# Kernel tuning notes

Hardware: AMD Instinct MI355X
Metric: run time of the kernel (lower is better)

Reference implementation:

```python
import jax, jax.numpy as jnp
import numpy as np

N, E, NS, NB = 25000, 400000, 4, 8
S0, V0 = 64, 32            # input: 64x0e + 32x1o
MS, MV = 96, 96            # message irreps: 96x0e + 96x1o
OS, OV = 128, 32           # post-linear_down/skip: (64+64)x0e + 32x1o
NIRR = S0 + V0             # node_feats.irreps.num_irreps = 96
AVG_NEIGH = 16.0
Y1 = float(np.sqrt(3.0 / (4.0 * np.pi)))  # integral-normalized l=1 SH coeff


def setup_inputs() -> dict:
    key = jax.random.key(0)
    k = jax.random.split(key, 15)
    return {
        'node_feats': jax.random.normal(k[0], (N, S0 + 3 * V0), jnp.float32),
        'vectors': jax.random.normal(k[1], (E, 3), jnp.float32),
        'rbf': jax.random.uniform(k[2], (E, NB), jnp.float32),
        'species': jax.random.randint(k[3], (N,), 0, NS, jnp.int32),
        'senders': jax.random.randint(k[4], (E,), 0, N, jnp.int32),
        'receivers': jax.random.randint(k[5], (E,), 0, N, jnp.int32),
        'W_up_s': jax.random.normal(k[6], (S0, S0), jnp.float32),
        'W_up_v': jax.random.normal(k[7], (V0, V0), jnp.float32),
        'W_mlp1': jax.random.normal(k[8], (NB, 64), jnp.float32),
        'W_mlp2': jax.random.normal(k[9], (64, 64), jnp.float32),
        'W_mlp3': jax.random.normal(k[10], (64, MS + MV), jnp.float32),
        'W_down_s': jax.random.normal(k[11], (MS, OS), jnp.float32),
        'W_down_v': jax.random.normal(k[12], (MV, OV), jnp.float32),
        'W_skip_s': jax.random.normal(k[13], (NS, S0, OS), jnp.float32),
        'W_skip_v': jax.random.normal(k[14], (NS, V0, OV), jnp.float32),
    }


def reference(node_feats, vectors, rbf, species, senders, receivers,
              W_up_s, W_up_v, W_mlp1, W_mlp2, W_mlp3,
              W_down_s, W_down_v, W_skip_s, W_skip_v):
    n = node_feats.shape[0]
    s = node_feats[:, :S0]                      # [N, 64]   0e
    v = node_feats[:, S0:].reshape(n, V0, 3)    # [N, 32,3] 1o

    # linear_up (per-irrep linear, 1/sqrt(fan_in) path normalization), then gather
    s_up = (s @ W_up_s) * (1.0 / jnp.sqrt(S0))
    v_up = jnp.einsum('nci,cd->ndi', v, W_up_v) * (1.0 / jnp.sqrt(V0))
    s_e = s_up[senders]                         # [E, 64]
    v_e = v_up[senders]                         # [E, 32, 3]

    # spherical harmonics l=1, normalize=True, 'integral' normalization
    y = Y1 * vectors / (jnp.linalg.norm(vectors, axis=-1, keepdims=True) + 1e-12)

    # tensor products filtered to output irreps + 0e
    tp_v = s_e[:, :, None] * y[:, None, :]                       # 0e x 1o -> 1o [E,64,3]
    tp_s = jnp.einsum('eci,ei->ec', v_e, y) * (1.0 / jnp.sqrt(3.0))  # 1o x 1o -> 0e [E,32]
    msg_s = jnp.concatenate([s_e, tp_s], axis=1)                 # [E, 96]
    msg_v = jnp.concatenate([v_e, tp_v], axis=1)                 # [E, 96, 3]

    # radial MLP -> per-edge, per-irrep mixing weights
    h = jax.nn.silu(rbf @ W_mlp1 * (1.0 / jnp.sqrt(NB)))
    h = jax.nn.silu(h @ W_mlp2 * (1.0 / 8.0))
    mix = h @ W_mlp3 * (1.0 / 8.0)                               # [E, 192]

    inv = 1.0 / NIRR
    msg_s = msg_s * mix[:, :MS] * inv
    msg_v = msg_v * (mix[:, MS:] * inv)[:, :, None]

    # scatter-sum to receivers, then normalize by sqrt(avg_num_neighbors)
    agg_s = jax.ops.segment_sum(msg_s, receivers, num_segments=n) / jnp.sqrt(AVG_NEIGH)
    agg_v = jax.ops.segment_sum(msg_v, receivers, num_segments=n) / jnp.sqrt(AVG_NEIGH)

    # linear_down to 128x0e + 32x1o
    out_s = agg_s @ W_down_s * (1.0 / jnp.sqrt(MS))
    out_v = jnp.einsum('nci,cd->ndi', agg_v, W_down_v) * (1.0 / jnp.sqrt(MV))

    # species-indexed skip connection (indexed linear)
    skip_s = jnp.einsum('nc,ncd->nd', s, W_skip_s[species]) * (1.0 / jnp.sqrt(S0))
    skip_v = jnp.einsum('nci,ncd->ndi', v, W_skip_v[species]) * (1.0 / jnp.sqrt(V0))

    f_s = out_s + skip_s                                         # [N, 128]
    f_v = out_v + skip_v                                         # [N, 32, 3]

    # equivariant gate: first 96 scalars activated, last 32 scalars gate the vectors
    act_s = jax.nn.silu(f_s[:, :OS - OV])
    gates = jax.nn.silu(f_s[:, OS - OV:])
    gated_v = f_v * gates[:, :, None]
    return jnp.concatenate([act_s, gated_v.reshape(n, OV * 3)], axis=1)  # [N, 192]
```

## Files before the change

kernel.cpp:

```cpp
#include <hip/hip_runtime.h>
#include <hip/hip_bf16.h>
#include <hip/hip_fp16.h>
#include <hip/hip_fp8.h>

#define NN 25000
#define EE 400000

#define SC_UP_S 0.125f
#define SC_UP_V 0.17677669529663689f
#define Y1C 0.48860251190291992f
#define SC_MLP1 0.35355339059327373f
#define SC_MLP2 0.125f
#define SC3 0.0013020833333333333f
#define INV_SQRT3 0.57735026918962584f
#define SC_DOWN 0.025515518153991442f
#define SC_SKIP_S 0.125f
#define SC_SKIP_V 0.17677669529663689f

typedef __attribute__((ext_vector_type(8))) short short8;
typedef __attribute__((ext_vector_type(4))) float f32x4;

__device__ __forceinline__ float silu(float x) {
  return __fdividef(x, 1.f + __expf(-x));
}
__device__ __forceinline__ unsigned short f2bf(float f) {
  unsigned u = __float_as_uint(f);
  unsigned r = u + 0x7FFF + ((u >> 16) & 1);
  return (unsigned short)(r >> 16);
}
__device__ __forceinline__ float bf2f(unsigned short s) {
  return __uint_as_float(((unsigned)s) << 16);
}
__device__ __forceinline__ float bfe(short8 v, int idx) {
  return __uint_as_float(((unsigned)(unsigned short)v[idx]) << 16);
}
__device__ __forceinline__ unsigned packbf(float lo, float hi) {
  return ((unsigned)f2bf(hi) << 16) | (unsigned)f2bf(lo);
}
__device__ __forceinline__ unsigned char f2fp8(float x) {
  __hip_fp8_e4m3 v(x);
  return (unsigned char)v.__x;
}
__device__ __forceinline__ float fp82f(unsigned b) {
  __hip_fp8_e4m3 t;
  t.__x = (__hip_fp8_storage_t)b;
  return (float)t;
}

#define W_W1P 0
#define W_W2P 1024
#define W_W3B 3072
#define W_WDS 9216
#define W_WDV 15360
#define W_SUPB 16896
#define W_VUPB (W_SUPB + NN * 32)
#define W_DEG (W_VUPB + NN * 48)
#define W_PRE (W_DEG + NN)
#define W_CUR (W_PRE + NN + 8)
#define W_SRT (W_CUR + NN)
#define W_EDN (W_SRT + EE * 2)
#define W_END (W_EDN + EE * 56)

__global__ __launch_bounds__(256) void transpose_weights(
    const float* __restrict__ W1, const float* __restrict__ W2,
    const float* __restrict__ W3, const float* __restrict__ Wds,
    const float* __restrict__ Wdv, float* __restrict__ ws) {
  int t = blockIdx.x * 256 + threadIdx.x;
  int stride = gridDim.x * 256;
  unsigned short* W1p = (unsigned short*)(ws + W_W1P);
  unsigned short* W2p = (unsigned short*)(ws + W_W2P);
  unsigned short* W3b = (unsigned short*)(ws + W_W3B);
  unsigned short* Wdsb = (unsigned short*)(ws + W_WDS);
  unsigned short* Wdvb = (unsigned short*)(ws + W_WDV);
  for (int i = t; i < 2048; i += stride) {
    int c = i >> 5, k = i & 31;
    W1p[i] = (k < 8) ? f2bf(W1[k * 64 + c] * SC_MLP1) : (unsigned short)0;
  }
  for (int i = t; i < 4096; i += stride) {
    int c = i >> 6, k = i & 63;
    W2p[i] = f2bf(W2[k * 64 + c] * SC_MLP2);
  }
  for (int i = t; i < 12288; i += stride) {
    int c = i >> 6, k = i & 63;
    float sc = (c >= 64 && c < 96) ? (SC3 * INV_SQRT3) : SC3;
    W3b[i] = f2bf(W3[k * 192 + c] * sc);
  }
  for (int i = t; i < 12288; i += stride) {
    int o = i / 96, k = i - 96 * o;
    Wdsb[i] = f2bf(Wds[k * 128 + o] * SC_DOWN);
  }
  for (int i = t; i < 3072; i += stride) {
    int o = i / 96, k = i - 96 * o;
    Wdvb[i] = f2bf(Wdv[k * 32 + o] * SC_DOWN);
  }
}

__global__ __launch_bounds__(256) void up_kernel(
    const float* __restrict__ nf, const float* __restrict__ Wus,
    const float* __restrict__ Wuv, unsigned short* __restrict__ s_upb,
    unsigned short* __restrict__ v_upb) {
  int n = blockIdx.x;
  int t = threadIdx.x;
  __shared__ float sv[160];
  if (t < 160) sv[t] = nf[n * 160 + t];
  __syncthreads();
  if (t < 64) {
    float a = 0.f;
#pragma unroll
    for (int k = 0; k < 64; k++) a += sv[k] * Wus[k * 64 + t];
    s_upb[n * 64 + t] = f2bf(a * SC_UP_S);
  } else if (t < 160) {
    int j = t - 64;
    int c = j / 3, i = j - 3 * c;
    float a = 0.f;
#pragma unroll
    for (int k = 0; k < 32; k++) a += sv[64 + k * 3 + i] * Wuv[k * 32 + c];
    v_upb[n * 96 + j] = f2bf(a * SC_UP_V);
  }
}

__global__ __launch_bounds__(256) void count_deg(
    const int* __restrict__ receivers, int* __restrict__ deg) {
  int e = blockIdx.x * 256 + threadIdx.x;
  if (e < EE) atomicAdd(&deg[receivers[e]], 1);
}

__global__ __launch_bounds__(1024) void scan_kernel(
    const int* __restrict__ deg, int* __restrict__ prefix,
    int* __restrict__ cursor) {
  __shared__ int waveSums[16];
  __shared__ int sCarry;
  int t = threadIdx.x;
  int lane = t & 63, wv = t >> 6;
  if (t == 0) sCarry = 0;
  __syncthreads();
  for (int base = 0; base < NN; base += 1024) {
    int i = base + t;
    int x = (i < NN) ? deg[i] : 0;
    int v = x;
#pragma unroll
    for (int d = 1; d < 64; d <<= 1) {
      int u = __shfl_up(v, d, 64);
      if (lane >= d) v += u;
    }
    if (lane == 63) waveSums[wv] = v;
    __syncthreads();
    if (wv == 0 && lane < 16) {
      int s = waveSums[lane];
#pragma unroll
      for (int d = 1; d < 16; d <<= 1) {
        int u = __shfl_up(s, d, 64);
        if (lane >= d) s += u;
      }
      waveSums[lane] = s;
    }
    __syncthreads();
    int waveOff = (wv == 0) ? 0 : waveSums[wv - 1];
    int incl = v + waveOff + sCarry;
    if (i < NN) {
      prefix[i] = incl - x;
      cursor[i] = incl - x;
    }
    __syncthreads();
    if (t == 1023) sCarry = incl;
    __syncthreads();
  }
  if (t == 0) prefix[NN] = sCarry;
}

__global__ __launch_bounds__(256) void scatter_kernel(
    const int* __restrict__ senders, const int* __restrict__ receivers,
    int* __restrict__ cursor, int2* __restrict__ sorted) {
  int e = blockIdx.x * 256 + threadIdx.x;
  if (e < EE) {
    int r = receivers[e];
    int pos = atomicAdd(&cursor[r], 1);
    sorted[pos] = make_int2(e, senders[e]);
  }
}

__global__ __launch_bounds__(256, 4) void edge_down3(
    const float* __restrict__ rbf, const float* __restrict__ vectors,
    const int2* __restrict__ sorted,
    const unsigned short* __restrict__ W1p,
    const unsigned short* __restrict__ W2p,
    const unsigned short* __restrict__ W3b,
    const unsigned short* __restrict__ Wdsb,
    const unsigned short* __restrict__ Wdvb,
    const unsigned short* __restrict__ s_upb,
    const unsigned short* __restrict__ v_upb,
    unsigned char* __restrict__ edown) {
  __shared__ unsigned short sH[64 * 72];
  __shared__ unsigned short sMix[64 * 200];

  int t = threadIdx.x;
  int pbase = blockIdx.x * 64;
  int lane = t & 63;
  int wv = t >> 6;
  int rl = lane & 15;
  int kgrp = lane >> 4;
  int arow = 16 * wv + rl;
  int crow = 16 * wv + kgrp * 4;

  union S8 { short8 v; unsigned u[4]; };

  int2 es = sorted[pbase + arow];
  int eid = es.x, snd = es.y;
  const unsigned short* seb = s_upb + (size_t)snd * 64;
  const unsigned short* veb = v_upb + (size_t)snd * 96;
  short8 se0 = *(const short8*)&seb[kgrp * 8];
  short8 se1 = *(const short8*)&seb[32 + kgrp * 8];
  short8 ve0 = *(const short8*)&veb[24 * kgrp];
  short8 ve1 = *(const short8*)&veb[24 * kgrp + 8];
  short8 ve2 = *(const short8*)&veb[24 * kgrp + 16];
  float vx = vectors[(size_t)eid * 3 + 0];
  float vy = vectors[(size_t)eid * 3 + 1];
  float vz = vectors[(size_t)eid * 3 + 2];
  float nrm = sqrtf(vx * vx + vy * vy + vz * vz) + 1e-12f;
  float ysc = Y1C / nrm;
  float y0 = vx * ysc, y1 = vy * ysc, y2 = vz * ysc;

  S8 a1;
  a1.u[0] = a1.u[1] = a1.u[2] = a1.u[3] = 0u;
  if (kgrp == 0) {
    float4 ra = *(const float4*)(rbf + (size_t)eid * 8);
    float4 rb = *(const float4*)(rbf + (size_t)eid * 8 + 4);
    a1.u[0] = packbf(ra.x, ra.y);
    a1.u[1] = packbf(ra.z, ra.w);
    a1.u[2] = packbf(rb.x, rb.y);
    a1.u[3] = packbf(rb.z, rb.w);
  }
#pragma unroll
  for (int ct = 0; ct < 4; ct++) {
    short8 b = *(const short8*)&W1p[(ct * 16 + rl) * 32 + kgrp * 8];
    f32x4 acc = {0.f, 0.f, 0.f, 0.f};
    acc = __builtin_amdgcn_mfma_f32_16x16x32_bf16(a1.v, b, acc, 0, 0, 0);
#pragma unroll
    for (int rr = 0; rr < 4; rr++)
      sH[(crow + rr) * 72 + ct * 16 + rl] = f2bf(silu(acc[rr]));
  }

  {
    short8 a20 = *(const short8*)&sH[arow * 72 + kgrp * 8];
    short8 a21 = *(const short8*)&sH[arow * 72 + 32 + kgrp * 8];
#pragma unroll
    for (int ct = 0; ct < 4; ct++) {
      const unsigned short* wb = &W2p[(ct * 16 + rl) * 64];
      short8 b0 = *(const short8*)&wb[kgrp * 8];
      short8 b1 = *(const short8*)&wb[32 + kgrp * 8];
      f32x4 acc = {0.f, 0.f, 0.f, 0.f};
      acc = __builtin_amdgcn_mfma_f32_16x16x32_bf16(a20, b0, acc, 0, 0, 0);
      acc = __builtin_amdgcn_mfma_f32_16x16x32_bf16(a21, b1, acc, 0, 0, 0);
#pragma unroll
      for (int rr = 0; rr < 4; rr++)
        sH[(crow + rr) * 72 + ct * 16 + rl] = f2bf(silu(acc[rr]));
    }
  }

  {
    short8 a30 = *(const short8*)&sH[arow * 72 + kgrp * 8];
    short8 a31 = *(const short8*)&sH[arow * 72 + 32 + kgrp * 8];
#pragma unroll
    for (int nt = 0; nt < 12; nt++) {
      int cc = nt * 16 + rl;
      const unsigned short* wb = &W3b[cc * 64];
      short8 b0 = *(const short8*)&wb[kgrp * 8];
      short8 b1 = *(const short8*)&wb[32 + kgrp * 8];
      f32x4 acc = {0.f, 0.f, 0.f, 0.f};
      acc = __builtin_amdgcn_mfma_f32_16x16x32_bf16(a30, b0, acc, 0, 0, 0);
      acc = __builtin_amdgcn_mfma_f32_16x16x32_bf16(a31, b1, acc, 0, 0, 0);
#pragma unroll
      for (int rr = 0; rr < 4; rr++)
        sMix[(crow + rr) * 200 + cc] = f2bf(acc[rr]);
    }
  }

  const unsigned short* mrow = &sMix[arow * 200];
  S8 as0, as1, as2, mvp1, mvp2, mvp3;
  {
    short8 m = *(const short8*)&mrow[kgrp * 8];
#pragma unroll
    for (int q = 0; q < 4; q++)
      as0.u[q] = packbf(bfe(se0, 2 * q) * bfe(m, 2 * q),
                        bfe(se0, 2 * q + 1) * bfe(m, 2 * q + 1));
  }
  {
    short8 m = *(const short8*)&mrow[32 + kgrp * 8];
#pragma unroll
    for (int q = 0; q < 4; q++)
      as1.u[q] = packbf(bfe(se1, 2 * q) * bfe(m, 2 * q),
                        bfe(se1, 2 * q + 1) * bfe(m, 2 * q + 1));
  }
  {
    short8 m = *(const short8*)&mrow[64 + kgrp * 8];
#pragma unroll
    for (int q = 0; q < 4; q++) {
      float d0 = bfe(ve0, (6 * q) % 8 == 6 * q ? 6 * q : 6 * q) * 0.f;
      (void)d0;
      float e0, e1, e2, f0, f1, f2;
      if (6 * q < 8) e0 = bfe(ve0, 6 * q); else if (6 * q < 16) e0 = bfe(ve1, 6 * q - 8); else e0 = bfe(ve2, 6 * q - 16);
      if (6 * q + 1 < 8) e1 = bfe(ve0, 6 * q + 1); else if (6 * q + 1 < 16) e1 = bfe(ve1, 6 * q - 7); else e1 = bfe(ve2, 6 * q - 15);
      if (6 * q + 2 < 8) e2 = bfe(ve0, 6 * q + 2); else if (6 * q + 2 < 16) e2 = bfe(ve1, 6 * q - 6); else e2 = bfe(ve2, 6 * q - 14);
      if (6 * q + 3 < 8) f0 = bfe(ve0, 6 * q + 3); else if (6 * q + 3 < 16) f0 = bfe(ve1, 6 * q - 5); else f0 = bfe(ve2, 6 * q - 13);
      if (6 * q + 4 < 8) f1 = bfe(ve0, 6 * q + 4); else if (6 * q + 4 < 16) f1 = bfe(ve1, 6 * q - 4); else f1 = bfe(ve2, 6 * q - 12);
      if (6 * q + 5 < 8) f2 = bfe(ve0, 6 * q + 5); else if (6 * q + 5 < 16) f2 = bfe(ve1, 6 * q - 3); else f2 = bfe(ve2, 6 * q - 11);
      float da = e0 * y0 + e1 * y1 + e2 * y2;
      float db = f0 * y0 + f1 * y1 + f2 * y2;
      as2.u[q] = packbf(da * bfe(m, 2 * q), db * bfe(m, 2 * q + 1));
    }
  }
  mvp1.v = *(const short8*)&mrow[96 + kgrp * 8];
  mvp2.v = *(const short8*)&mrow[128 + kgrp * 8];
  mvp3.v = *(const short8*)&mrow[160 + kgrp * 8];
  __syncthreads();

  unsigned char* edL = (unsigned char*)sMix;
#pragma unroll
  for (int ot = 0; ot < 8; ot++) {
    int col = ot * 16 + rl;
    const unsigned short* wb = &Wdsb[col * 96];
    short8 b0 = *(const short8*)&wb[kgrp * 8];
    short8 b1 = *(const short8*)&wb[32 + kgrp * 8];
    short8 b2 = *(const short8*)&wb[64 + kgrp * 8];
    f32x4 acc = {0.f, 0.f, 0.f, 0.f};
    acc = __builtin_amdgcn_mfma_f32_16x16x32_bf16(as0.v, b0, acc, 0, 0, 0);
    acc = __builtin_amdgcn_mfma_f32_16x16x32_bf16(as1.v, b1, acc, 0, 0, 0);
    acc = __builtin_amdgcn_mfma_f32_16x16x32_bf16(as2.v, b2, acc, 0, 0, 0);
#pragma unroll
    for (int rr = 0; rr < 4; rr++)
      edL[(crow + rr) * 232 + col] = f2fp8(acc[rr]);
  }
  float yarr[3] = {y0, y1, y2};
#pragma unroll
  for (int i = 0; i < 3; i++) {
    S8 av0, av1, av2;
#pragma unroll
    for (int q = 0; q < 4; q++) {
      float g0, g1;
      {
        const int j0 = 0;
        (void)j0;
      }
      int ja = 6 * q + i, jb = 6 * q + 3 + i;
      if (ja < 8) g0 = bfe(ve0, ja); else if (ja < 16) g0 = bfe(ve1, ja - 8); else g0 = bfe(ve2, ja - 16);
      if (jb < 8) g1 = bfe(ve0, jb); else if (jb < 16) g1 = bfe(ve1, jb - 8); else g1 = bfe(ve2, jb - 16);
      av0.u[q] = packbf(g0 * bfe(mvp1.v, 2 * q), g1 * bfe(mvp1.v, 2 * q + 1));
      av1.u[q] = packbf(bfe(se0, 2 * q) * yarr[i] * bfe(mvp2.v, 2 * q),
                        bfe(se0, 2 * q + 1) * yarr[i] * bfe(mvp2.v, 2 * q + 1));
      av2.u[q] = packbf(bfe(se1, 2 * q) * yarr[i] * bfe(mvp3.v, 2 * q),
                        bfe(se1, 2 * q + 1) * yarr[i] * bfe(mvp3.v, 2 * q + 1));
    }
#pragma unroll
    for (int ot = 0; ot < 2; ot++) {
      int o = ot * 16 + rl;
      const unsigned short* wb = &Wdvb[o * 96];
      short8 b0 = *(const short8*)&wb[kgrp * 8];
      short8 b1 = *(const short8*)&wb[32 + kgrp * 8];
      short8 b2 = *(const short8*)&wb[64 + kgrp * 8];
      f32x4 acc = {0.f, 0.f, 0.f, 0.f};
      acc = __builtin_amdgcn_mfma_f32_16x16x32_bf16(av0.v, b0, acc, 0, 0, 0);
      acc = __builtin_amdgcn_mfma_f32_16x16x32_bf16(av1.v, b1, acc, 0, 0, 0);
      acc = __builtin_amdgcn_mfma_f32_16x16x32_bf16(av2.v, b2, acc, 0, 0, 0);
#pragma unroll
      for (int rr = 0; rr < 4; rr++)
        edL[(crow + rr) * 232 + 128 + o * 3 + i] = f2fp8(acc[rr]);
    }
  }
  __syncthreads();

  {
    int row = t >> 2, q = t & 3;
    const unsigned* src = (const unsigned*)(edL + row * 232 + q * 56);
    unsigned* dst = (unsigned*)(edown + (size_t)(pbase + row) * 224 + q * 56);
#pragma unroll
    for (int j = 0; j < 14; j++) dst[j] = src[j];
  }
}

__global__ __launch_bounds__(256) void gather_out3(
    const float* __restrict__ nf, const int* __restrict__ species,
    const int* __restrict__ prefix, const unsigned* __restrict__ edw,
    const float* __restrict__ Wss, const float* __restrict__ Wsv,
    float* __restrict__ out) {
  int n = blockIdx.x;
  int t = threadIdx.x;
  __shared__ float sNF[160];
  __shared__ float4 sPart[4][56];
  __shared__ float sEd[224];
  __shared__ float sF[224];
  if (t < 160) sNF[t] = nf[(size_t)n * 160 + t];
  int beg = prefix[n], end = prefix[n + 1];
  if (t < 224) {
    int u = t % 56, rg = t / 56;
    float a0 = 0.f, a1 = 0.f, a2 = 0.f, a3 = 0.f;
    for (int s = beg + rg; s < end; s += 4) {
      unsigned v = edw[(size_t)s * 56 + u];
      a0 += fp82f(v & 0xFF);
      a1 += fp82f((v >> 8) & 0xFF);
      a2 += fp82f((v >> 16) & 0xFF);
      a3 += fp82f(v >> 24);
    }
    sPart[rg][u] = make_float4(a0, a1, a2, a3);
  }
  __syncthreads();
  if (t < 56) {
    float4 a = sPart[0][t], b = sPart[1][t], c = sPart[2][t], d = sPart[3][t];
    sEd[4 * t + 0] = a.x + b.x + c.x + d.x;
    sEd[4 * t + 1] = a.y + b.y + c.y + d.y;
    sEd[4 * t + 2] = a.z + b.z + c.z + d.z;
    sEd[4 * t + 3] = a.w + b.w + c.w + d.w;
  }
  __syncthreads();
  int spec = species[n];
  if (t < 128) {
    const float* wsk = Wss + (size_t)spec * 64 * 128;
    float b = 0.f;
#pragma unroll
    for (int k = 0; k < 64; k++) b += sNF[k] * wsk[k * 128 + t];
    sF[t] = sEd[t] + b * SC_SKIP_S;
  } else if (t < 224) {
    int j = t - 128;
    int c = j / 3, i = j - 3 * c;
    const float* wsk = Wsv + (size_t)spec * 32 * 32;
    float b = 0.f;
#pragma unroll
    for (int k = 0; k < 32; k++) b += sNF[64 + k * 3 + i] * wsk[k * 32 + c];
    sF[t] = sEd[t] + b * SC_SKIP_V;
  }
  __syncthreads();
  if (t < 96) {
    out[(size_t)n * 192 + t] = silu(sF[t]);
  } else if (t < 192) {
    int j = t - 96;
    int c = j / 3;
    out[(size_t)n * 192 + t] = sF[128 + j] * silu(sF[96 + c]);
  }
}

extern "C" void kernel_launch(void* const* d_in, const int* in_sizes, int n_in,
                              void* d_out, int out_size, void* d_ws, size_t ws_size,
                              hipStream_t stream) {
  const float* nf = (const float*)d_in[0];
  const float* vectors = (const float*)d_in[1];
  const float* rbf = (const float*)d_in[2];
  const int* species = (const int*)d_in[3];
  const int* senders = (const int*)d_in[4];
  const int* receivers = (const int*)d_in[5];
  const float* Wus = (const float*)d_in[6];
  const float* Wuv = (const float*)d_in[7];
  const float* W1 = (const float*)d_in[8];
  const float* W2 = (const float*)d_in[9];
  const float* W3 = (const float*)d_in[10];
  const float* Wds = (const float*)d_in[11];
  const float* Wdv = (const float*)d_in[12];
  const float* Wss = (const float*)d_in[13];
  const float* Wsv = (const float*)d_in[14];

  float* ws = (float*)d_ws;
  const unsigned short* W1p = (const unsigned short*)(ws + W_W1P);
  const unsigned short* W2p = (const unsigned short*)(ws + W_W2P);
  const unsigned short* W3b = (const unsigned short*)(ws + W_W3B);
  const unsigned short* Wdsb = (const unsigned short*)(ws + W_WDS);
  const unsigned short* Wdvb = (const unsigned short*)(ws + W_WDV);
  unsigned short* s_upb = (unsigned short*)(ws + W_SUPB);
  unsigned short* v_upb = (unsigned short*)(ws + W_VUPB);
  int* deg = (int*)(ws + W_DEG);
  int* prefix = (int*)(ws + W_PRE);
  int* cursor = (int*)(ws + W_CUR);
  int2* sorted = (int2*)(ws + W_SRT);
  unsigned char* edown = (unsigned char*)(ws + W_EDN);
  float* out = (float*)d_out;

  transpose_weights<<<16, 256, 0, stream>>>(W1, W2, W3, Wds, Wdv, ws);
  up_kernel<<<NN, 256, 0, stream>>>(nf, Wus, Wuv, s_upb, v_upb);

  hipMemsetAsync(deg, 0, (size_t)NN * sizeof(int), stream);
  count_deg<<<(EE + 255) / 256, 256, 0, stream>>>(receivers, deg);
  scan_kernel<<<1, 1024, 0, stream>>>(deg, prefix, cursor);
  scatter_kernel<<<(EE + 255) / 256, 256, 0, stream>>>(senders, receivers,
                                                       cursor, sorted);
  edge_down3<<<EE / 64, 256, 0, stream>>>(rbf, vectors, sorted, W1p, W2p, W3b,
                                          Wdsb, Wdvb, s_upb, v_upb, edown);
  gather_out3<<<NN, 256, 0, stream>>>(nf, species, prefix, (const unsigned*)edown,
                                      Wss, Wsv, out);
}
```

Before: 355.9 us.

## Process edges in original order and scatter results by receiver rank

```diff
diff --git a/kernel.cpp b/kernel.cpp
--- a/kernel.cpp
+++ b/kernel.cpp
@@ -24,9 +24,8 @@
   return __fdividef(x, 1.f + __expf(-x));
 }
 __device__ __forceinline__ unsigned short f2bf(float f) {
-  unsigned u = __float_as_uint(f);
-  unsigned r = u + 0x7FFF + ((u >> 16) & 1);
-  return (unsigned short)(r >> 16);
+  __hip_bfloat16 h = __float2bfloat16(f);
+  return *reinterpret_cast<unsigned short*>(&h);
 }
 __device__ __forceinline__ float bf2f(unsigned short s) {
   return __uint_as_float(((unsigned)s) << 16);
@@ -52,19 +51,22 @@
 #define W_W3B 3072
 #define W_WDS 9216
 #define W_WDV 15360
-#define W_SUPB 16896
+#define W_WSS 16896
+#define W_WSV 33280
+#define W_SUPB 35328
 #define W_VUPB (W_SUPB + NN * 32)
 #define W_DEG (W_VUPB + NN * 48)
 #define W_PRE (W_DEG + NN)
 #define W_CUR (W_PRE + NN + 8)
-#define W_SRT (W_CUR + NN)
-#define W_EDN (W_SRT + EE * 2)
+#define W_RNK (W_CUR + NN)
+#define W_EDN (W_RNK + EE)
 #define W_END (W_EDN + EE * 56)
 
 __global__ __launch_bounds__(256) void transpose_weights(
     const float* __restrict__ W1, const float* __restrict__ W2,
     const float* __restrict__ W3, const float* __restrict__ Wds,
-    const float* __restrict__ Wdv, float* __restrict__ ws) {
+    const float* __restrict__ Wdv, const float* __restrict__ Wss,
+    const float* __restrict__ Wsv, float* __restrict__ ws) {
   int t = blockIdx.x * 256 + threadIdx.x;
   int stride = gridDim.x * 256;
   unsigned short* W1p = (unsigned short*)(ws + W_W1P);
@@ -72,6 +74,8 @@
   unsigned short* W3b = (unsigned short*)(ws + W_W3B);
   unsigned short* Wdsb = (unsigned short*)(ws + W_WDS);
   unsigned short* Wdvb = (unsigned short*)(ws + W_WDV);
+  unsigned short* Wssb = (unsigned short*)(ws + W_WSS);
+  unsigned short* Wsvb = (unsigned short*)(ws + W_WSV);
   for (int i = t; i < 2048; i += stride) {
     int c = i >> 5, k = i & 31;
     W1p[i] = (k < 8) ? f2bf(W1[k * 64 + c] * SC_MLP1) : (unsigned short)0;
@@ -93,6 +97,10 @@
     int o = i / 96, k = i - 96 * o;
     Wdvb[i] = f2bf(Wdv[k * 32 + o] * SC_DOWN);
   }
+  for (int i = t; i < 32768; i += stride)
+    Wssb[i] = f2bf(Wss[i] * SC_SKIP_S);
+  for (int i = t; i < 4096; i += stride)
+    Wsvb[i] = f2bf(Wsv[i] * SC_SKIP_V);
 }
 
 __global__ __launch_bounds__(256) void up_kernel(
@@ -168,20 +176,19 @@
   if (t == 0) prefix[NN] = sCarry;
 }
 
-__global__ __launch_bounds__(256) void scatter_kernel(
-    const int* __restrict__ senders, const int* __restrict__ receivers,
-    int* __restrict__ cursor, int2* __restrict__ sorted) {
+__global__ __launch_bounds__(256) void rank_kernel(
+    const int* __restrict__ receivers, int* __restrict__ cursor,
+    int* __restrict__ rankArr) {
   int e = blockIdx.x * 256 + threadIdx.x;
   if (e < EE) {
     int r = receivers[e];
-    int pos = atomicAdd(&cursor[r], 1);
-    sorted[pos] = make_int2(e, senders[e]);
-  }
-}
-
-__global__ __launch_bounds__(256, 4) void edge_down3(
+    rankArr[e] = atomicAdd(&cursor[r], 1);
+  }
+}
+
+__global__ __launch_bounds__(256, 4) void edge_down4(
     const float* __restrict__ rbf, const float* __restrict__ vectors,
-    const int2* __restrict__ sorted,
+    const int* __restrict__ senders, const int* __restrict__ rankArr,
     const unsigned short* __restrict__ W1p,
     const unsigned short* __restrict__ W2p,
     const unsigned short* __restrict__ W3b,
@@ -192,6 +199,7 @@
     unsigned char* __restrict__ edown) {
   __shared__ unsigned short sH[64 * 72];
   __shared__ unsigned short sMix[64 * 200];
+  __shared__ int sRank[64];
 
   int t = threadIdx.x;
   int pbase = blockIdx.x * 64;
@@ -204,8 +212,9 @@
 
   union S8 { short8 v; unsigned u[4]; };
 
-  int2 es = sorted[pbase + arow];
-  int eid = es.x, snd = es.y;
+  if (t < 64) sRank[t] = rankArr[pbase + t];
+  int eid = pbase + arow;
+  int snd = senders[eid];
   const unsigned short* seb = s_upb + (size_t)snd * 64;
   const unsigned short* veb = v_upb + (size_t)snd * 96;
   short8 se0 = *(const short8*)&seb[kgrp * 8];
@@ -295,8 +304,6 @@
     short8 m = *(const short8*)&mrow[64 + kgrp * 8];
 #pragma unroll
     for (int q = 0; q < 4; q++) {
-      float d0 = bfe(ve0, (6 * q) % 8 == 6 * q ? 6 * q : 6 * q) * 0.f;
-      (void)d0;
       float e0, e1, e2, f0, f1, f2;
       if (6 * q < 8) e0 = bfe(ve0, 6 * q); else if (6 * q < 16) e0 = bfe(ve1, 6 * q - 8); else e0 = bfe(ve2, 6 * q - 16);
       if (6 * q + 1 < 8) e1 = bfe(ve0, 6 * q + 1); else if (6 * q + 1 < 16) e1 = bfe(ve1, 6 * q - 7); else e1 = bfe(ve2, 6 * q - 15);
@@ -337,10 +344,6 @@
 #pragma unroll
     for (int q = 0; q < 4; q++) {
       float g0, g1;
-      {
-        const int j0 = 0;
-        (void)j0;
-      }
       int ja = 6 * q + i, jb = 6 * q + 3 + i;
       if (ja < 8) g0 = bfe(ve0, ja); else if (ja < 16) g0 = bfe(ve1, ja - 8); else g0 = bfe(ve2, ja - 16);
       if (jb < 8) g1 = bfe(ve0, jb); else if (jb < 16) g1 = bfe(ve1, jb - 8); else g1 = bfe(ve2, jb - 16);
@@ -371,61 +374,68 @@
   {
     int row = t >> 2, q = t & 3;
     const unsigned* src = (const unsigned*)(edL + row * 232 + q * 56);
-    unsigned* dst = (unsigned*)(edown + (size_t)(pbase + row) * 224 + q * 56);
+    unsigned* dst = (unsigned*)(edown + (size_t)sRank[row] * 224 + q * 56);
 #pragma unroll
     for (int j = 0; j < 14; j++) dst[j] = src[j];
   }
 }
 
-__global__ __launch_bounds__(256) void gather_out3(
+__global__ __launch_bounds__(256) void gather_out4(
     const float* __restrict__ nf, const int* __restrict__ species,
-    const int* __restrict__ prefix, const unsigned* __restrict__ edw,
-    const float* __restrict__ Wss, const float* __restrict__ Wsv,
-    float* __restrict__ out) {
+    const int* __restrict__ prefix, const unsigned char* __restrict__ edown,
+    const unsigned short* __restrict__ Wssb,
+    const unsigned short* __restrict__ Wsvb, float* __restrict__ out) {
   int n = blockIdx.x;
   int t = threadIdx.x;
   __shared__ float sNF[160];
-  __shared__ float4 sPart[4][56];
+  __shared__ float sPart[16 * 224];
   __shared__ float sEd[224];
   __shared__ float sF[224];
   if (t < 160) sNF[t] = nf[(size_t)n * 160 + t];
   int beg = prefix[n], end = prefix[n + 1];
   if (t < 224) {
-    int u = t % 56, rg = t / 56;
-    float a0 = 0.f, a1 = 0.f, a2 = 0.f, a3 = 0.f;
-    for (int s = beg + rg; s < end; s += 4) {
-      unsigned v = edw[(size_t)s * 56 + u];
-      a0 += fp82f(v & 0xFF);
-      a1 += fp82f((v >> 8) & 0xFF);
-      a2 += fp82f((v >> 16) & 0xFF);
-      a3 += fp82f(v >> 24);
-    }
-    sPart[rg][u] = make_float4(a0, a1, a2, a3);
-  }
-  __syncthreads();
-  if (t < 56) {
-    float4 a = sPart[0][t], b = sPart[1][t], c = sPart[2][t], d = sPart[3][t];
-    sEd[4 * t + 0] = a.x + b.x + c.x + d.x;
-    sEd[4 * t + 1] = a.y + b.y + c.y + d.y;
-    sEd[4 * t + 2] = a.z + b.z + c.z + d.z;
-    sEd[4 * t + 3] = a.w + b.w + c.w + d.w;
+    int u = t % 14, rg = t / 14;
+    float a[16];
+#pragma unroll
+    for (int j = 0; j < 16; j++) a[j] = 0.f;
+    for (int s = beg + rg; s < end; s += 16) {
+      uint4 v = *(const uint4*)(edown + (size_t)s * 224 + u * 16);
+      unsigned w[4] = {v.x, v.y, v.z, v.w};
+#pragma unroll
+      for (int p = 0; p < 4; p++) {
+        a[4 * p + 0] += fp82f(w[p] & 0xFF);
+        a[4 * p + 1] += fp82f((w[p] >> 8) & 0xFF);
+        a[4 * p + 2] += fp82f((w[p] >> 16) & 0xFF);
+        a[4 * p + 3] += fp82f(w[p] >> 24);
+      }
+    }
+#pragma unroll
+    for (int j = 0; j < 16; j += 4)
+      *(float4*)&sPart[rg * 224 + u * 16 + j] = *(float4*)&a[j];
+  }
+  __syncthreads();
+  if (t < 224) {
+    float s = 0.f;
+#pragma unroll
+    for (int rg = 0; rg < 16; rg++) s += sPart[rg * 224 + t];
+    sEd[t] = s;
   }
   __syncthreads();
   int spec = species[n];
   if (t < 128) {
-    const float* wsk = Wss + (size_t)spec * 64 * 128;
+    const unsigned short* wsk = Wssb + (size_t)spec * 8192;
     float b = 0.f;
 #pragma unroll
-    for (int k = 0; k < 64; k++) b += sNF[k] * wsk[k * 128 + t];
-    sF[t] = sEd[t] + b * SC_SKIP_S;
+    for (int k = 0; k < 64; k++) b += sNF[k] * bf2f(wsk[k * 128 + t]);
+    sF[t] = sEd[t] + b;
   } else if (t < 224) {
     int j = t - 128;
     int c = j / 3, i = j - 3 * c;
-    const float* wsk = Wsv + (size_t)spec * 32 * 32;
+    const unsigned short* wsk = Wsvb + (size_t)spec * 1024;
     float b = 0.f;
 #pragma unroll
-    for (int k = 0; k < 32; k++) b += sNF[64 + k * 3 + i] * wsk[k * 32 + c];
-    sF[t] = sEd[t] + b * SC_SKIP_V;
+    for (int k = 0; k < 32; k++) b += sNF[64 + k * 3 + i] * bf2f(wsk[k * 32 + c]);
+    sF[t] = sEd[t] + b;
   }
   __syncthreads();
   if (t < 96) {
@@ -462,25 +472,27 @@
   const unsigned short* W3b = (const unsigned short*)(ws + W_W3B);
   const unsigned short* Wdsb = (const unsigned short*)(ws + W_WDS);
   const unsigned short* Wdvb = (const unsigned short*)(ws + W_WDV);
+  const unsigned short* Wssb = (const unsigned short*)(ws + W_WSS);
+  const unsigned short* Wsvb = (const unsigned short*)(ws + W_WSV);
   unsigned short* s_upb = (unsigned short*)(ws + W_SUPB);
   unsigned short* v_upb = (unsigned short*)(ws + W_VUPB);
   int* deg = (int*)(ws + W_DEG);
   int* prefix = (int*)(ws + W_PRE);
   int* cursor = (int*)(ws + W_CUR);
-  int2* sorted = (int2*)(ws + W_SRT);
+  int* rankArr = (int*)(ws + W_RNK);
   unsigned char* edown = (unsigned char*)(ws + W_EDN);
   float* out = (float*)d_out;
 
-  transpose_weights<<<16, 256, 0, stream>>>(W1, W2, W3, Wds, Wdv, ws);
+  transpose_weights<<<16, 256, 0, stream>>>(W1, W2, W3, Wds, Wdv, Wss, Wsv, ws);
   up_kernel<<<NN, 256, 0, stream>>>(nf, Wus, Wuv, s_upb, v_upb);
 
   hipMemsetAsync(deg, 0, (size_t)NN * sizeof(int), stream);
   count_deg<<<(EE + 255) / 256, 256, 0, stream>>>(receivers, deg);
   scan_kernel<<<1, 1024, 0, stream>>>(deg, prefix, cursor);
-  scatter_kernel<<<(EE + 255) / 256, 256, 0, stream>>>(senders, receivers,
-                                                       cursor, sorted);
-  edge_down3<<<EE / 64, 256, 0, stream>>>(rbf, vectors, sorted, W1p, W2p, W3b,
-                                          Wdsb, Wdvb, s_upb, v_upb, edown);
-  gather_out3<<<NN, 256, 0, stream>>>(nf, species, prefix, (const unsigned*)edown,
-                                      Wss, Wsv, out);
-}
+  rank_kernel<<<(EE + 255) / 256, 256, 0, stream>>>(receivers, cursor, rankArr);
+  edge_down4<<<EE / 64, 256, 0, stream>>>(rbf, vectors, senders, rankArr, W1p,
+                                          W2p, W3b, Wdsb, Wdvb, s_upb, v_upb,
+                                          edown);
+  gather_out4<<<NN, 256, 0, stream>>>(nf, species, prefix, edown, Wssb, Wsvb,
+                                      out);
+}
```

After: 349.3 us. Within noise of the previous version (-1.9%).
